# Optimization experiments

Hardware: AMD Instinct MI355X
Metric: run time of the kernel (lower is better)

The kernel has to match this reference:

```python
import jax, jax.numpy as jnp
import numpy as np

P = 7       # patch (window) size
H_HEADS = 8
D_HEAD = 64
SCALE = D_HEAD ** -0.5


def setup_inputs() -> dict:
    key = jax.random.key(0)
    k1, k2, k3, k4 = jax.random.split(key, 4)
    dim, inner = 256, H_HEADS * D_HEAD
    fmap = jax.random.normal(k1, (32, 56, 56, dim), dtype=jnp.float32)
    Wq = jax.random.normal(k2, (dim, inner), dtype=jnp.float32) * (dim ** -0.5)
    Wkv = jax.random.normal(k3, (dim, 2 * inner), dtype=jnp.float32) * (dim ** -0.5)
    Wo = jax.random.normal(k4, (inner, dim), dtype=jnp.float32) * (inner ** -0.5)
    bo = jnp.zeros((dim,), dtype=jnp.float32)
    return {"fmap": fmap, "Wq": Wq, "Wkv": Wkv, "Wo": Wo, "bo": bo}


def reference(fmap, Wq, Wkv, Wo, bo):
    b, X, Y, c = fmap.shape
    x, y = X // P, Y // P
    h, d = H_HEADS, D_HEAD
    # window partition: b (x p1) (y p2) c -> (b x y) p1 p2 c
    f = fmap.reshape(b, x, P, y, P, c).transpose(0, 1, 3, 2, 4, 5)
    f = f.reshape(b * x * y, P, P, c)
    # 1x1 convs == matmul over channels
    q = f @ Wq                       # (B, p, p, h*d)
    k_, v = jnp.split(f @ Wkv, 2, axis=-1)
    B = b * x * y
    pp = P * P
    def to_heads(t):  # (B,p,p,h*d) -> (B,h,pp,d)
        return t.reshape(B, pp, h, d).transpose(0, 2, 1, 3)
    q, k_, v = map(to_heads, (q, k_, v))
    dots = jnp.einsum('bhid,bhjd->bhij', q, k_) * SCALE
    attn = jax.nn.softmax(dots, axis=-1)
    out = jnp.einsum('bhij,bhjd->bhid', attn, v)      # (B,h,pp,d)
    # (b x y h) (p1 p2) d -> b (x p1) (y p2) (h d)
    out = out.reshape(b, x, y, h, P, P, d)
    out = out.transpose(0, 1, 4, 2, 5, 3, 6).reshape(b, X, Y, h * d)
    return out @ Wo + bo
```

## Files before the change

### kernel.cpp

```cpp
#include <hip/hip_runtime.h>
#include <hip/hip_bf16.h>

typedef __bf16 bf16;
typedef __bf16 bf16x4 __attribute__((ext_vector_type(4)));
typedef __bf16 bf16x8 __attribute__((ext_vector_type(8)));
typedef float f32x4 __attribute__((ext_vector_type(4)));

#define TOK 100352
#define ATT_SCALE 0.125f

#define GLOAD_LDS16(g, l)                                                        \
  __builtin_amdgcn_global_load_lds((const __attribute__((address_space(1))) void*)(g), \
                                   (__attribute__((address_space(3))) void*)(l), 16, 0, 0)

__global__ __launch_bounds__(256) void transpose_cast_k(const float* __restrict__ in,
                                                        bf16* __restrict__ out, int R, int C) {
  __shared__ float t[32][33];
  int c0 = blockIdx.x * 32, r0 = blockIdx.y * 32;
  int tx = threadIdx.x, ty = threadIdx.y;
#pragma unroll
  for (int i = ty; i < 32; i += 8)
    t[i][tx] = in[(size_t)(r0 + i) * C + c0 + tx];
  __syncthreads();
#pragma unroll
  for (int i = ty; i < 32; i += 8)
    out[(size_t)(c0 + i) * R + r0 + tx] = (bf16)t[tx][i];
}

__global__ __launch_bounds__(256) void qkvg_k(const float* __restrict__ fmap,
                                              const bf16* __restrict__ Bt,
                                              bf16* __restrict__ qkv2,
                                              bf16* __restrict__ Vtg, int wbase0) {
  __shared__ bf16 Bs[2][128 * 64];
  const int tid = threadIdx.x;
  const int lane = tid & 63, wv = tid >> 6;
  const int l15 = lane & 15, l4 = lane >> 4;
  const int g = blockIdx.x;
  const int blk = blockIdx.y;
  bf16x8 af[2][8];
  int wl[2], tt[2];
#pragma unroll
  for (int m = 0; m < 2; ++m) {
    int tokl = blk * 128 + wv * 32 + m * 16 + l15;
    int w = tokl / 49, t = tokl - w * 49;
    wl[m] = w; tt[m] = t;
    int wg = wbase0 + w;
    int p1 = t / 7, p2 = t - p1 * 7;
    const float* ab = fmap +
        (size_t)((((wg >> 6) * 56) + ((wg >> 3) & 7) * 7 + p1) * 56 + (wg & 7) * 7 + p2) * 256;
#pragma unroll
    for (int j = 0; j < 8; ++j) {
      const float* p = ab + j * 32 + l4 * 8;
      float4 f0 = *(const float4*)p;
      float4 f1 = *(const float4*)(p + 4);
      bf16x8 o;
      o[0] = (bf16)f0.x; o[1] = (bf16)f0.y; o[2] = (bf16)f0.z; o[3] = (bf16)f0.w;
      o[4] = (bf16)f1.x; o[5] = (bf16)f1.y; o[6] = (bf16)f1.z; o[7] = (bf16)f1.w;
      af[m][j] = o;
    }
  }
  const int sg = lane >> 3;
  const int scol = ((lane & 7) ^ (sg & 7)) * 8;
#define STAGE_B(tt_, buf_)                                                                   \
  do {                                                                                       \
    int bn_ = g * 4 + ((tt_) >> 2), ks_ = (tt_) & 3;                                         \
    _Pragma("unroll") for (int i_ = 0; i_ < 4; ++i_)                                         \
        GLOAD_LDS16(Bt + (size_t)(bn_ * 128 + wv * 32 + i_ * 8 + sg) * 256 + ks_ * 64 + scol,\
                    Bs[buf_] + wv * 2048 + i_ * 512);                                        \
  } while (0)

  f32x4 acc[2][8] = {};
  STAGE_B(0, 0);
  __syncthreads();
#pragma unroll
  for (int t = 0; t < 16; ++t) {
    const int cur = t & 1, ks = t & 3;
    if (t < 15) STAGE_B(t + 1, cur ^ 1);
#pragma unroll
    for (int kk = 0; kk < 2; ++kk) {
      bf16x8 bfr[8];
#pragma unroll
      for (int n = 0; n < 8; ++n) {
        int rv = n * 16 + l15;
        bfr[n] = *(const bf16x8*)((const char*)Bs[cur] +
                 ((rv * 128 + kk * 64 + l4 * 16) ^ ((rv & 7) << 4)));
      }
#pragma unroll
      for (int m = 0; m < 2; ++m)
#pragma unroll
        for (int n = 0; n < 8; ++n)
          acc[m][n] = __builtin_amdgcn_mfma_f32_16x16x32_bf16(bfr[n], af[m][ks * 2 + kk],
                                                              acc[m][n], 0, 0, 0);
    }
    if (ks == 3) {
      const int bn = g * 4 + (t >> 2);
      if (g < 2) {
#pragma unroll
        for (int m = 0; m < 2; ++m) {
          size_t row = (size_t)blk * 128 + wv * 32 + m * 16 + l15;
#pragma unroll
          for (int n = 0; n < 8; ++n) {
            bf16x4 pk;
#pragma unroll
            for (int r = 0; r < 4; ++r) pk[r] = (bf16)acc[m][n][r];
            *(bf16x4*)(qkv2 + row * 1024 + bn * 128 + n * 16 + l4 * 4) = pk;
          }
        }
      } else {
#pragma unroll
        for (int m = 0; m < 2; ++m) {
#pragma unroll
          for (int n = 0; n < 8; ++n) {
            int d0 = (bn - 8) * 128 + n * 16 + l4 * 4;
            int h = d0 >> 6, dd = d0 & 63;
            size_t vb = ((size_t)wl[m] * 8 + h) * 4096 + (size_t)dd * 64 + tt[m];
#pragma unroll
            for (int r = 0; r < 4; ++r) Vtg[vb + (size_t)r * 64] = (bf16)acc[m][n][r];
          }
        }
      }
#pragma unroll
      for (int m = 0; m < 2; ++m)
#pragma unroll
        for (int n = 0; n < 8; ++n) acc[m][n] = (f32x4){0.f, 0.f, 0.f, 0.f};
    }
    __syncthreads();
  }
#undef STAGE_B
}

__global__ __launch_bounds__(256) void attn2_k(const bf16* __restrict__ qkv2,
                                               const bf16* __restrict__ Vtg,
                                               const bf16* __restrict__ Wo_t,
                                               const float* __restrict__ bias,
                                               float* __restrict__ out, int wbase) {
  __shared__ bf16 Qs[64 * 64], Ks[64 * 64], Vt[64 * 64], Ps[4 * 16 * 64], HO[64 * 64];
  const int w = blockIdx.x;
  const int tid = threadIdx.x, lane = tid & 63, wv = tid >> 6;
  const int l15 = lane & 15, l4 = lane >> 4;
  const size_t bqk = (size_t)w * 49 * 1024;
  const bf16* vbase = Vtg + (size_t)w * 8 * 4096;
  const int wg = wbase + w;
  char* pbase = (char*)Ps + wv * 2048;
  const int sr = wv * 8 + (lane >> 3);
  const int scc = ((lane & 7) ^ ((lane >> 3) & 7)) * 8;
  f32x4 acco[4][4] = {};
  for (int h = 0; h < 8; ++h) {
#pragma unroll
    for (int i = 0; i < 2; ++i) {
      GLOAD_LDS16(qkv2 + bqk + (size_t)(i * 32 + sr) * 1024 + h * 64 + scc,
                  Qs + i * 2048 + wv * 512);
      GLOAD_LDS16(qkv2 + bqk + (size_t)(i * 32 + sr) * 1024 + 512 + h * 64 + scc,
                  Ks + i * 2048 + wv * 512);
      GLOAD_LDS16(vbase + (size_t)h * 4096 + (i * 32 + sr) * 64 + scc,
                  Vt + i * 2048 + wv * 512);
    }
    __syncthreads();
    f32x4 s[4] = {};
#pragma unroll
    for (int kk = 0; kk < 2; ++kk) {
      int rq = wv * 16 + l15;
      bf16x8 aq = *(const bf16x8*)((const char*)Qs +
                  ((rq * 128 + kk * 64 + l4 * 16) ^ ((rq & 7) << 4)));
#pragma unroll
      for (int n = 0; n < 4; ++n) {
        int rk = n * 16 + l15;
        bf16x8 bk = *(const bf16x8*)((const char*)Ks +
                    ((rk * 128 + kk * 64 + l4 * 16) ^ ((rk & 7) << 4)));
        s[n] = __builtin_amdgcn_mfma_f32_16x16x32_bf16(aq, bk, s[n], 0, 0, 0);
      }
    }
    float pr[4][4];
#pragma unroll
    for (int reg = 0; reg < 4; ++reg) {
      float m = -1e30f;
#pragma unroll
      for (int n = 0; n < 4; ++n) {
        float v = s[n][reg] * ATT_SCALE;
        if (n * 16 + l15 < 49) m = fmaxf(m, v);
      }
#pragma unroll
      for (int d = 1; d < 16; d <<= 1) m = fmaxf(m, __shfl_xor(m, d));
      float sum = 0.f;
#pragma unroll
      for (int n = 0; n < 4; ++n) {
        float p = (n * 16 + l15 < 49) ? __expf(s[n][reg] * ATT_SCALE - m) : 0.f;
        pr[n][reg] = p;
        sum += p;
      }
#pragma unroll
      for (int d = 1; d < 16; d <<= 1) sum += __shfl_xor(sum, d);
      float inv = 1.f / sum;
#pragma unroll
      for (int n = 0; n < 4; ++n) pr[n][reg] *= inv;
    }
#pragma unroll
    for (int n = 0; n < 4; ++n)
#pragma unroll
      for (int reg = 0; reg < 4; ++reg) {
        int rl = l4 * 4 + reg, col = n * 16 + l15;
        int off = ((rl * 64 + col) * 2) ^ ((rl & 7) << 4);
        *(bf16*)(pbase + off) = (bf16)pr[n][reg];
      }
    f32x4 o[4] = {};
#pragma unroll
    for (int kk = 0; kk < 2; ++kk) {
      int rp = l15;
      bf16x8 ap = *(const bf16x8*)(pbase +
                  ((rp * 128 + kk * 64 + l4 * 16) ^ ((rp & 7) << 4)));
#pragma unroll
      for (int n = 0; n < 4; ++n) {
        int rv = n * 16 + l15;
        bf16x8 bv = *(const bf16x8*)((const char*)Vt +
                    ((rv * 128 + kk * 64 + l4 * 16) ^ ((rv & 7) << 4)));
        o[n] = __builtin_amdgcn_mfma_f32_16x16x32_bf16(bv, ap, o[n], 0, 0, 0);
      }
    }
    {
      int hrow = wv * 16 + l15;
#pragma unroll
      for (int n = 0; n < 4; ++n) {
        bf16x4 pk;
#pragma unroll
        for (int r = 0; r < 4; ++r) pk[r] = (bf16)o[n][r];
        int off = (hrow * 128 + n * 32 + l4 * 8) ^ ((hrow & 7) << 4);
        *(bf16x4*)((char*)HO + off) = pk;
      }
    }
    __syncthreads();
#pragma unroll
    for (int kk = 0; kk < 2; ++kk) {
      bf16x8 af[4];
#pragma unroll
      for (int m = 0; m < 4; ++m) {
        int r = m * 16 + l15;
        af[m] = *(const bf16x8*)((const char*)HO +
                 ((r * 128 + kk * 64 + l4 * 16) ^ ((r & 7) << 4)));
      }
#pragma unroll
      for (int n = 0; n < 4; ++n) {
        int wr = wv * 64 + n * 16 + l15;
        bf16x8 bv = *(const bf16x8*)(Wo_t + (size_t)wr * 512 + h * 64 + kk * 32 + l4 * 8);
#pragma unroll
        for (int m = 0; m < 4; ++m)
          acco[m][n] = __builtin_amdgcn_mfma_f32_16x16x32_bf16(bv, af[m], acco[m][n], 0, 0, 0);
      }
    }
  }
  int bb = wg >> 6, xx = (wg >> 3) & 7, yy = wg & 7;
#pragma unroll
  for (int m = 0; m < 4; ++m) {
    int rl = m * 16 + l15;
    if (rl < 49) {
      int p1 = rl / 7, p2 = rl - p1 * 7;
      size_t orow = (size_t)(bb * 56 + xx * 7 + p1) * 56 + yy * 7 + p2;
      float* op = out + orow * 256 + wv * 64;
#pragma unroll
      for (int n = 0; n < 4; ++n) {
        int col = n * 16 + l4 * 4;
        float4 b4 = *(const float4*)(bias + wv * 64 + col);
        float4 v;
        v.x = acco[m][n][0] + b4.x;
        v.y = acco[m][n][1] + b4.y;
        v.z = acco[m][n][2] + b4.z;
        v.w = acco[m][n][3] + b4.w;
        *(float4*)(op + col) = v;
      }
    }
  }
}

extern "C" void kernel_launch(void* const* d_in, const int* in_sizes, int n_in,
                              void* d_out, int out_size, void* d_ws, size_t ws_size,
                              hipStream_t stream) {
  const float* fmap = (const float*)d_in[0];
  const float* Wq = (const float*)d_in[1];
  const float* Wkv = (const float*)d_in[2];
  const float* Wo = (const float*)d_in[3];
  const float* bo = (const float*)d_in[4];
  float* out = (float*)d_out;
  char* ws = (char*)d_ws;

  const size_t WQKV_B = 1536ull * 256 * 2;
  const size_t WO_B = 256ull * 512 * 2;
  const size_t wbytes = WQKV_B + WO_B;

  int nc = 0;
  size_t Tc = 0, VtgB = 0;
  for (int c = 2; c <= 16; c <<= 1) {
    size_t tc = TOK / c;
    size_t vb = (tc / 49) * 65536ull;
    if (wbytes + vb + tc * 2048ull + 65536ull <= ws_size) { nc = c; Tc = tc; VtgB = vb; break; }
  }
  if (nc == 0) return;

  bf16* Wqkv_t = (bf16*)(ws);
  bf16* Wo_t = (bf16*)(ws + WQKV_B);
  bf16* Vtg = (bf16*)(ws + wbytes);
  bf16* qkv2 = (bf16*)(ws + wbytes + VtgB);

  hipMemsetAsync(Vtg, 0, VtgB, stream);

  hipLaunchKernelGGL(transpose_cast_k, dim3(16, 8), dim3(32, 8), 0, stream, Wq, Wqkv_t, 256, 512);
  hipLaunchKernelGGL(transpose_cast_k, dim3(32, 8), dim3(32, 8), 0, stream, Wkv,
                     Wqkv_t + 512 * 256, 256, 1024);
  hipLaunchKernelGGL(transpose_cast_k, dim3(8, 16), dim3(32, 8), 0, stream, Wo, Wo_t, 512, 256);

  for (int c = 0; c < nc; ++c) {
    int tok0 = (int)(c * Tc);
    int wloc = (int)(Tc / 49);
    hipLaunchKernelGGL(qkvg_k, dim3(3, (int)(Tc / 128)), dim3(256), 0, stream, fmap, Wqkv_t,
                       qkv2, Vtg, tok0 / 49);
    hipLaunchKernelGGL(attn2_k, dim3(wloc), dim3(256), 0, stream, qkv2, Vtg, Wo_t, bo, out,
                       tok0 / 49);
  }
}
```

Measured before the change: 344.4 us.

## Double-buffer K/V tiles across heads and load Q directly from global

In the attention kernel, K and V tiles for the next head are prefetched into a second LDS buffer while the current head computes, replacing the load-then-wait pattern each iteration. Q fragments are now read straight from global memory into registers instead of being staged through LDS, which frees that buffer. This is meant to hide global-to-LDS latency per head, at the cost of more LDS for the doubled K/V buffers (possibly lowering occupancy) and direct global loads of Q on the critical path. Q rows beyond 49 are read from neighbouring windows' memory, as before via LDS.

```diff
diff --git a/kernel.cpp b/kernel.cpp
--- a/kernel.cpp
+++ b/kernel.cpp
@@ -134,7 +134,7 @@
                                                const bf16* __restrict__ Wo_t,
                                                const float* __restrict__ bias,
                                                float* __restrict__ out, int wbase) {
-  __shared__ bf16 Qs[64 * 64], Ks[64 * 64], Vt[64 * 64], Ps[4 * 16 * 64], HO[64 * 64];
+  __shared__ bf16 Ks[2][64 * 64], Vt[2][64 * 64], Ps[4 * 16 * 64], HO[64 * 64];
   const int w = blockIdx.x;
   const int tid = threadIdx.x, lane = tid & 63, wv = tid >> 6;
   const int l15 = lane & 15, l4 = lane >> 4;
@@ -144,30 +144,39 @@
   char* pbase = (char*)Ps + wv * 2048;
   const int sr = wv * 8 + (lane >> 3);
   const int scc = ((lane & 7) ^ ((lane >> 3) & 7)) * 8;
+#pragma unroll
+  for (int i = 0; i < 2; ++i) {
+    GLOAD_LDS16(qkv2 + bqk + (size_t)(i * 32 + sr) * 1024 + 512 + scc,
+                Ks[0] + i * 2048 + wv * 512);
+    GLOAD_LDS16(vbase + (size_t)(i * 32 + sr) * 64 + scc, Vt[0] + i * 2048 + wv * 512);
+  }
   f32x4 acco[4][4] = {};
   for (int h = 0; h < 8; ++h) {
-#pragma unroll
-    for (int i = 0; i < 2; ++i) {
-      GLOAD_LDS16(qkv2 + bqk + (size_t)(i * 32 + sr) * 1024 + h * 64 + scc,
-                  Qs + i * 2048 + wv * 512);
-      GLOAD_LDS16(qkv2 + bqk + (size_t)(i * 32 + sr) * 1024 + 512 + h * 64 + scc,
-                  Ks + i * 2048 + wv * 512);
-      GLOAD_LDS16(vbase + (size_t)h * 4096 + (i * 32 + sr) * 64 + scc,
-                  Vt + i * 2048 + wv * 512);
-    }
+    const int cur = h & 1;
     __syncthreads();
+    if (h < 7) {
+#pragma unroll
+      for (int i = 0; i < 2; ++i) {
+        GLOAD_LDS16(qkv2 + bqk + (size_t)(i * 32 + sr) * 1024 + 512 + (h + 1) * 64 + scc,
+                    Ks[cur ^ 1] + i * 2048 + wv * 512);
+        GLOAD_LDS16(vbase + (size_t)(h + 1) * 4096 + (i * 32 + sr) * 64 + scc,
+                    Vt[cur ^ 1] + i * 2048 + wv * 512);
+      }
+    }
+    const int rq = wv * 16 + l15;
+    bf16x8 aq[2];
+#pragma unroll
+    for (int kk = 0; kk < 2; ++kk)
+      aq[kk] = *(const bf16x8*)(qkv2 + bqk + (size_t)rq * 1024 + h * 64 + kk * 32 + l4 * 8);
     f32x4 s[4] = {};
 #pragma unroll
     for (int kk = 0; kk < 2; ++kk) {
-      int rq = wv * 16 + l15;
-      bf16x8 aq = *(const bf16x8*)((const char*)Qs +
-                  ((rq * 128 + kk * 64 + l4 * 16) ^ ((rq & 7) << 4)));
 #pragma unroll
       for (int n = 0; n < 4; ++n) {
         int rk = n * 16 + l15;
-        bf16x8 bk = *(const bf16x8*)((const char*)Ks +
+        bf16x8 bk = *(const bf16x8*)((const char*)Ks[cur] +
                     ((rk * 128 + kk * 64 + l4 * 16) ^ ((rk & 7) << 4)));
-        s[n] = __builtin_amdgcn_mfma_f32_16x16x32_bf16(aq, bk, s[n], 0, 0, 0);
+        s[n] = __builtin_amdgcn_mfma_f32_16x16x32_bf16(aq[kk], bk, s[n], 0, 0, 0);
       }
     }
     float pr[4][4];
@@ -211,7 +220,7 @@
 #pragma unroll
       for (int n = 0; n < 4; ++n) {
         int rv = n * 16 + l15;
-        bf16x8 bv = *(const bf16x8*)((const char*)Vt +
+        bf16x8 bv = *(const bf16x8*)((const char*)Vt[cur] +
                     ((rv * 128 + kk * 64 + l4 * 16) ^ ((rv & 7) << 4)));
         o[n] = __builtin_amdgcn_mfma_f32_16x16x32_bf16(bv, ap, o[n], 0, 0, 0);
       }
```

Measured after the change: 358.1 us. 4.0% more time.
